# Kernel tuning notes

Measured on AMD Instinct MI355X. Metric: run time of the kernel, lower is better.

Reference implementation:

```python
import jax, jax.numpy as jnp
import numpy as np

N = 50000
E = 800000
D_IN = 128
D_HID = 512
D_OUT = 128
BN_EPS = 1e-5


def setup_inputs() -> dict:
    key = jax.random.key(0)
    ks = jax.random.split(key, 12)
    inp = {}
    inp["v"] = jax.random.normal(ks[0], (N, D_IN), dtype=jnp.float32)
    inp["src"] = jax.random.randint(ks[1], (E,), 0, N, dtype=jnp.int32)
    inp["dst"] = jax.random.randint(ks[2], (E,), 0, N, dtype=jnp.int32)
    inp["edge_weight"] = jax.random.uniform(ks[3], (E,), dtype=jnp.float32)
    # learned parameters
    inp["epsilon"] = jnp.zeros((1, 1), dtype=jnp.float32)  # nn.Parameter([[0.0]])
    s1 = 1.0 / np.sqrt(D_IN)
    s2 = 1.0 / np.sqrt(D_HID)
    inp["W1"] = jax.random.uniform(ks[4], (D_IN, D_HID), minval=-s1, maxval=s1, dtype=jnp.float32)
    inp["b1"] = jax.random.uniform(ks[5], (D_HID,), minval=-s1, maxval=s1, dtype=jnp.float32)
    inp["gamma1"] = jnp.ones((D_HID,), dtype=jnp.float32)
    inp["beta1"] = jnp.zeros((D_HID,), dtype=jnp.float32)
    inp["W2"] = jax.random.uniform(ks[6], (D_HID, D_OUT), minval=-s2, maxval=s2, dtype=jnp.float32)
    inp["b2"] = jax.random.uniform(ks[7], (D_OUT,), minval=-s2, maxval=s2, dtype=jnp.float32)
    inp["gamma2"] = jnp.ones((D_OUT,), dtype=jnp.float32)
    inp["beta2"] = jnp.zeros((D_OUT,), dtype=jnp.float32)
    return inp


def _batchnorm(x, gamma, beta):
    # training-mode BN: batch mean / biased variance over the node axis
    mean = jnp.mean(x, axis=0)
    var = jnp.mean(jnp.square(x - mean), axis=0)
    return gamma * (x - mean) * jax.lax.rsqrt(var + BN_EPS) + beta


def reference(v, src, dst, edge_weight, epsilon, W1, b1, gamma1, beta1, W2, b2, gamma2, beta2):
    n = v.shape[0]
    # sparse.mm(a, v): out[dst] += w * v[src]
    msgs = v[src] * edge_weight[:, None]               # [E, D_IN]
    v_agg = jax.ops.segment_sum(msgs, dst, num_segments=n)  # [N, D_IN]
    v_agg = v_agg + epsilon * v                        # epsilon residual
    h = jax.nn.relu(_batchnorm(v_agg @ W1 + b1, gamma1, beta1))
    out = jax.nn.relu(_batchnorm(h @ W2 + b2, gamma2, beta2))
    return out
```

## Files before the change

### kernel.cpp

```cpp
#include <hip/hip_runtime.h>

#define N_NODES 50000
#define E_EDGES 800000
#define D_INF   128
#define D_HIDF  512
#define D_OUTF  128
#define SCAN_NB ((N_NODES + 255) / 256)
#define M1BLKS  ((N_NODES + 255) / 256)
#define FBLKS   ((N_NODES + 63) / 64)
#define EQ8     (E_EDGES / 8)

#define HIST_NB  ((EQ8 + 255) / 256)
#define CAST_NB  3125
#define PREPW_NB 256
#define PREP_ALL_NB (HIST_NB + CAST_NB + 2 * PREPW_NB)

typedef unsigned short u16;
typedef __attribute__((ext_vector_type(8))) short short8;
typedef __attribute__((ext_vector_type(4))) float floatx4;
typedef const __attribute__((address_space(1))) void gas_t;
typedef __attribute__((address_space(3))) void las_t;

__device__ __forceinline__ u16 f2bf(float f) {
    union { float f; unsigned u; } v; v.f = f;
    unsigned r = (v.u + 0x7fffu + ((v.u >> 16) & 1u)) >> 16;
    return (u16)r;
}
__device__ __forceinline__ float bf2f(u16 b) {
    union { unsigned u; float f; } v; v.u = ((unsigned)b) << 16; return v.f;
}

__global__ __launch_bounds__(256) void prep_all_kernel(
        const float* __restrict__ v, const float* __restrict__ W1,
        const float* __restrict__ W2, const int* __restrict__ dst,
        u16* __restrict__ vbf, u16* __restrict__ W1t, u16* __restrict__ W2t,
        int* __restrict__ counts, int* __restrict__ pos) {
    int b = blockIdx.x;
    int tid = threadIdx.x;
    if (b < HIST_NB) {
        int t = b * 256 + tid;
        if (t >= EQ8) return;
        int d[8], p[8];
#pragma unroll
        for (int k = 0; k < 8; ++k) d[k] = dst[t + k * EQ8];
#pragma unroll
        for (int k = 0; k < 8; ++k) p[k] = atomicAdd(&counts[d[k]], 1);
#pragma unroll
        for (int k = 0; k < 8; ++k) pos[t + k * EQ8] = p[k];
    } else if (b < HIST_NB + CAST_NB) {
        int i = (b - HIST_NB) * 256 + tid;
        const float4 a = ((const float4*)v)[i * 2];
        const float4 c = ((const float4*)v)[i * 2 + 1];
        u16 o[8];
        o[0] = f2bf(a.x); o[1] = f2bf(a.y); o[2] = f2bf(a.z); o[3] = f2bf(a.w);
        o[4] = f2bf(c.x); o[5] = f2bf(c.y); o[6] = f2bf(c.z); o[7] = f2bf(c.w);
        ((float4*)vbf)[i] = *(const float4*)o;
    } else if (b < HIST_NB + CAST_NB + PREPW_NB) {
        int idx = (b - HIST_NB - CAST_NB) * 256 + tid;
        int k1 = idx >> 9, n1 = idx & 511;
        W1t[n1 * 128 + k1] = f2bf(W1[idx]);
    } else {
        int idx = (b - HIST_NB - CAST_NB - PREPW_NB) * 256 + tid;
        int k2 = idx >> 7, n2 = idx & 127;
        W2t[n2 * 512 + k2] = f2bf(W2[idx]);
    }
}

__global__ __launch_bounds__(256) void reduce_kernel(const int* __restrict__ counts,
                                                     int* __restrict__ block_sums) {
    __shared__ int lsum[4];
    int tid = threadIdx.x;
    int gid = blockIdx.x * 256 + tid;
    int s = (gid < N_NODES) ? counts[gid] : 0;
#pragma unroll
    for (int off = 32; off; off >>= 1) s += __shfl_down(s, off);
    if ((tid & 63) == 0) lsum[tid >> 6] = s;
    __syncthreads();
    if (tid == 0) block_sums[blockIdx.x] = lsum[0] + lsum[1] + lsum[2] + lsum[3];
}

__global__ __launch_bounds__(256) void scan_final(const int* __restrict__ counts,
                                                  const int* __restrict__ block_sums,
                                                  int* __restrict__ row_start) {
    __shared__ int sh[256];
    __shared__ int bs[256];
    int tid = threadIdx.x;
    int gid = blockIdx.x * 256 + tid;
    sh[tid] = (gid < N_NODES) ? counts[gid] : 0;
    bs[tid] = (tid < SCAN_NB) ? block_sums[tid] : 0;
    __syncthreads();
    for (int off = 1; off < 256; off <<= 1) {
        int t1 = (tid >= off) ? sh[tid - off] : 0;
        int t2 = (tid >= off) ? bs[tid - off] : 0;
        __syncthreads();
        sh[tid] += t1;
        bs[tid] += t2;
        __syncthreads();
    }
    int boff = (blockIdx.x == 0) ? 0 : bs[blockIdx.x - 1];
    int excl = (tid == 0) ? 0 : sh[tid - 1];
    if (gid < N_NODES) row_start[gid] = boff + excl;
    if (gid == 0) row_start[N_NODES] = E_EDGES;
}

__global__ void fill_kernel(const int* __restrict__ src, const int* __restrict__ dst,
                            const float* __restrict__ w, const int* __restrict__ pos,
                            const int* __restrict__ row_start,
                            int2* __restrict__ csr_ew) {
    int e = blockIdx.x * blockDim.x + threadIdx.x;
    if (e >= E_EDGES) return;
    int d = dst[e];
    int idx = row_start[d] + pos[e];
    int2 rec;
    rec.x = src[e];
    rec.y = __float_as_int(w[e]);
    csr_ew[idx] = rec;
}

__global__ __launch_bounds__(256) void gather_kernel(const u16* __restrict__ vbf,
                                                     const int* __restrict__ row_start,
                                                     const int2* __restrict__ csr_ew,
                                                     const float* __restrict__ eps_p,
                                                     u16* __restrict__ vagg) {
    int node = blockIdx.x * 16 + (threadIdx.x >> 4);
    if (node >= N_NODES) return;
    int c8 = (threadIdx.x & 15) << 3;
    int beg = row_start[node];
    int end = row_start[node + 1];
    float a[8] = {};
    int j = beg;
    for (; j + 1 < end; j += 2) {
        int2 e0 = csr_ew[j];
        int2 e1 = csr_ew[j + 1];
        float w0 = __int_as_float(e0.y);
        float w1 = __int_as_float(e1.y);
        float4 r0 = *(const float4*)(vbf + (size_t)e0.x * D_INF + c8);
        float4 r1 = *(const float4*)(vbf + (size_t)e1.x * D_INF + c8);
        const u16* p0 = (const u16*)&r0;
        const u16* p1 = (const u16*)&r1;
#pragma unroll
        for (int t = 0; t < 8; ++t) a[t] += w0 * bf2f(p0[t]);
#pragma unroll
        for (int t = 0; t < 8; ++t) a[t] += w1 * bf2f(p1[t]);
    }
    if (j < end) {
        int2 e0 = csr_ew[j];
        float w0 = __int_as_float(e0.y);
        float4 r0 = *(const float4*)(vbf + (size_t)e0.x * D_INF + c8);
        const u16* p0 = (const u16*)&r0;
#pragma unroll
        for (int t = 0; t < 8; ++t) a[t] += w0 * bf2f(p0[t]);
    }
    float e = eps_p[0];
    float4 rn = *(const float4*)(vbf + (size_t)node * D_INF + c8);
    const u16* pn = (const u16*)&rn;
    u16 o[8];
#pragma unroll
    for (int t = 0; t < 8; ++t) o[t] = f2bf(a[t] + e * bf2f(pn[t]));
    *(float4*)(vagg + (size_t)node * D_INF + c8) = *(const float4*)o;
}

__global__ __launch_bounds__(512) void stats_gemm1(
        const u16* __restrict__ A, const u16* __restrict__ Bt,
        const float* __restrict__ bias,
        float* __restrict__ psum, float* __restrict__ psq, int M) {
    __shared__ __align__(16) char smem[24576];
    u16* As = (u16*)smem;
    u16* Bs = (u16*)(smem + 16384);
    const int bm = blockIdx.y * 256;
    const int bn = blockIdx.x * 128;
    const int tid = threadIdx.x;
    const int wave = tid >> 6, lane = tid & 63;
    const int wr = wave >> 1, wc = wave & 1;
    const int wm = wr * 64, wn = wc * 64;
    const int lm = lane & 15, quad = lane >> 4;
    floatx4 acc[4][4] = {};
    for (int ks = 0; ks < 4; ++ks) {
        const int k0 = ks << 5;
        {
            const int sub = lane >> 2, s = lane & 3;
#pragma unroll
            for (int t = 0; t < 3; ++t) {
                int ch = wave * 3 + t;
                if (ch < 16) {
                    int row = ch * 16 + sub;
                    int grow = bm + row; if (grow > M - 1) grow = M - 1;
                    int ss = s ^ (row & 3);
                    __builtin_amdgcn_global_load_lds(
                        (gas_t*)(A + (size_t)grow * 128 + k0 + ss * 8),
                        (las_t*)(As + row * 32 + s * 8), 16, 0, 0);
                } else {
                    int row = (ch - 16) * 16 + sub;
                    int ss = s ^ (row & 3);
                    __builtin_amdgcn_global_load_lds(
                        (gas_t*)(Bt + (size_t)(bn + row) * 128 + k0 + ss * 8),
                        (las_t*)(Bs + row * 32 + s * 8), 16, 0, 0);
                }
            }
        }
        __syncthreads();
        short8 af[4], bfr[4];
#pragma unroll
        for (int i = 0; i < 4; ++i) {
            int row = wm + i * 16 + lm;
            af[i] = *(const short8*)&As[row * 32 + ((quad ^ (row & 3)) * 8)];
        }
#pragma unroll
        for (int j = 0; j < 4; ++j) {
            int row = wn + j * 16 + lm;
            bfr[j] = *(const short8*)&Bs[row * 32 + ((quad ^ (row & 3)) * 8)];
        }
#pragma unroll
        for (int i = 0; i < 4; ++i)
#pragma unroll
            for (int j = 0; j < 4; ++j)
                acc[i][j] = __builtin_amdgcn_mfma_f32_16x16x32_bf16(af[i], bfr[j], acc[i][j], 0, 0, 0);
        __syncthreads();
    }
    float* redS = (float*)smem;
    float* redQ = redS + 128;
    if (tid < 128) { redS[tid] = 0.f; redQ[tid] = 0.f; }
    __syncthreads();
#pragma unroll
    for (int j = 0; j < 4; ++j) {
        int cl = wn + j * 16 + lm;
        float bj = bias[bn + cl];
        float s = 0.f, q = 0.f;
#pragma unroll
        for (int i = 0; i < 4; ++i) {
            int row0 = bm + wm + i * 16 + quad * 4;
#pragma unroll
            for (int r = 0; r < 4; ++r)
                if (row0 + r < M) { float x = acc[i][j][r] + bj; s += x; q += x * x; }
        }
        s += __shfl_xor(s, 16); q += __shfl_xor(q, 16);
        s += __shfl_xor(s, 32); q += __shfl_xor(q, 32);
        if (quad == 0) { atomicAdd(&redS[cl], s); atomicAdd(&redQ[cl], q); }
    }
    __syncthreads();
    if (tid < 128) {
        psum[(size_t)blockIdx.y * 512 + bn + tid] = redS[tid];
        psq [(size_t)blockIdx.y * 512 + bn + tid] = redQ[tid];
    }
}

__global__ __launch_bounds__(512, 4) void fused_mlp(
        const u16* __restrict__ vagg, const u16* __restrict__ W1t,
        const u16* __restrict__ W2t,
        const float* __restrict__ b1, const float* __restrict__ scale1,
        const float* __restrict__ shift1, const float* __restrict__ b2,
        u16* __restrict__ x2, float* __restrict__ psum, float* __restrict__ psq,
        int M) {
    __shared__ __align__(16) char smem[81920];
    u16* As  = (u16*)smem;
    u16* W1s = (u16*)(smem + 16384);
    u16* W2s = (u16*)smem;
    u16* hs  = (u16*)(smem + 16384);
    const int bm = blockIdx.x * 64;
    const int tid = threadIdx.x;
    const int wave = tid >> 6, lane = tid & 63;
    const int wr = wave >> 2, wc = wave & 3;
    const int wm = wr * 32;
    const int wn1 = wc * 128;
    const int wn2 = wc * 32;
    const int lm = lane & 15, quad = lane >> 4;

    floatx4 acc1[2][8] = {};
    floatx4 acc2[2][2] = {};

    auto stage_w1 = [&](int win) {
#pragma unroll
        for (int u = 0; u < 8; ++u) {
            int c = tid + u * 512;
            int col = c >> 3, s = c & 7;
            __builtin_amdgcn_global_load_lds(
                (gas_t*)(W1t + (size_t)col * 128 + win * 64 + ((s ^ (col & 7)) * 8)),
                (las_t*)(W1s + col * 64 + s * 8), 16, 0, 0);
        }
    };
    auto stage_w2 = [&](int win) {
#pragma unroll
        for (int u = 0; u < 2; ++u) {
            int c = tid + u * 512;
            int n = c >> 3, s = c & 7;
            __builtin_amdgcn_global_load_lds(
                (gas_t*)(W2t + (size_t)n * 512 + win * 64 + ((s ^ (n & 7)) * 8)),
                (las_t*)(W2s + n * 64 + s * 8), 16, 0, 0);
        }
    };
    auto compute1 = [&](int ks) {
        short8 a[2], b[8];
#pragma unroll
        for (int i = 0; i < 2; ++i) {
            int row = wm + i * 16 + lm;
            a[i] = *(const short8*)&As[row * 128 + (((ks * 4 + quad) ^ (row & 7)) * 8)];
        }
#pragma unroll
        for (int j = 0; j < 8; ++j) {
            int col = wn1 + j * 16 + lm;
            b[j] = *(const short8*)&W1s[col * 64 + ((((ks & 1) * 4 + quad) ^ (col & 7)) * 8)];
        }
#pragma unroll
        for (int i = 0; i < 2; ++i)
#pragma unroll
            for (int j = 0; j < 8; ++j)
                acc1[i][j] = __builtin_amdgcn_mfma_f32_16x16x32_bf16(a[i], b[j], acc1[i][j], 0, 0, 0);
    };
    auto compute2 = [&](int ks) {
        short8 a[2], b[2];
#pragma unroll
        for (int i = 0; i < 2; ++i) {
            int row = wm + i * 16 + lm;
            a[i] = *(const short8*)&hs[row * 512 + (((ks * 4 + quad) ^ (row & 7)) * 8)];
        }
#pragma unroll
        for (int j = 0; j < 2; ++j) {
            int n = wn2 + j * 16 + lm;
            b[j] = *(const short8*)&W2s[n * 64 + ((((ks & 1) * 4 + quad) ^ (n & 7)) * 8)];
        }
#pragma unroll
        for (int i = 0; i < 2; ++i)
#pragma unroll
            for (int j = 0; j < 2; ++j)
                acc2[i][j] = __builtin_amdgcn_mfma_f32_16x16x32_bf16(a[i], b[j], acc2[i][j], 0, 0, 0);
    };

#pragma unroll
    for (int u = 0; u < 2; ++u) {
        int c = tid + u * 512;
        int row = c >> 4, s = c & 15;
        int grow = bm + row; if (grow > M - 1) grow = M - 1;
        __builtin_amdgcn_global_load_lds(
            (gas_t*)(vagg + (size_t)grow * 128 + ((s ^ (row & 7)) * 8)),
            (las_t*)(As + row * 128 + s * 8), 16, 0, 0);
    }
    stage_w1(0);
    __syncthreads();
    compute1(0); compute1(1);
    __syncthreads();
    stage_w1(1);
    __syncthreads();
    compute1(2); compute1(3);
    __syncthreads();

    stage_w2(0);
    {
        float hsc[8], hsh[8];
#pragma unroll
        for (int j = 0; j < 8; ++j) {
            int col = wn1 + j * 16 + lm;
            float sc = scale1[col];
            hsc[j] = sc;
            hsh[j] = shift1[col] + sc * b1[col];
        }
#pragma unroll
        for (int i = 0; i < 2; ++i)
#pragma unroll
            for (int j = 0; j < 8; ++j)
#pragma unroll
                for (int r = 0; r < 4; ++r) {
                    int row = wm + i * 16 + quad * 4 + r;
                    int col = wn1 + j * 16 + lm;
                    float hv = fmaxf(0.f, acc1[i][j][r] * hsc[j] + hsh[j]);
                    hs[row * 512 + (((col >> 3) ^ (row & 7)) * 8) + (col & 7)] = f2bf(hv);
                }
    }
    __syncthreads();

#pragma unroll
    for (int win = 0; win < 8; ++win) {
        compute2(win * 2); compute2(win * 2 + 1);
        __syncthreads();
        if (win < 7) { stage_w2(win + 1); __syncthreads(); }
    }

    float* redS = (float*)smem;
    float* redQ = redS + 128;
    if (tid < 128) { redS[tid] = 0.f; redQ[tid] = 0.f; }
    __syncthreads();
    float bj2[2];
#pragma unroll
    for (int j = 0; j < 2; ++j) {
        int cl = wn2 + j * 16 + lm;
        bj2[j] = b2[cl];
        float s = 0.f, q = 0.f;
#pragma unroll
        for (int i = 0; i < 2; ++i) {
            int row0 = bm + wm + i * 16 + quad * 4;
#pragma unroll
            for (int r = 0; r < 4; ++r)
                if (row0 + r < M) { float x = acc2[i][j][r] + bj2[j]; s += x; q += x * x; }
        }
        s += __shfl_xor(s, 16); q += __shfl_xor(q, 16);
        s += __shfl_xor(s, 32); q += __shfl_xor(q, 32);
        if (quad == 0) { atomicAdd(&redS[cl], s); atomicAdd(&redQ[cl], q); }
    }
    __syncthreads();
    if (tid < 128) {
        psum[(size_t)blockIdx.x * 128 + tid] = redS[tid];
        psq [(size_t)blockIdx.x * 128 + tid] = redQ[tid];
    }
    __syncthreads();

    float* obuf = (float*)smem;
#pragma unroll
    for (int i = 0; i < 2; ++i)
#pragma unroll
        for (int j = 0; j < 2; ++j)
#pragma unroll
            for (int r = 0; r < 4; ++r) {
                int row = wm + i * 16 + quad * 4 + r;
                int col = wn2 + j * 16 + lm;
                obuf[row * 132 + col] = acc2[i][j][r] + bj2[j];
            }
    __syncthreads();
    {
        int row = tid >> 3, seg = (tid & 7) * 16;
        int grow = bm + row;
        if (grow < M) {
            u16 ob[16];
#pragma unroll
            for (int t = 0; t < 4; ++t) {
                float4 f = *(float4*)&obuf[row * 132 + seg + t * 4];
                ob[t * 4 + 0] = f2bf(f.x);
                ob[t * 4 + 1] = f2bf(f.y);
                ob[t * 4 + 2] = f2bf(f.z);
                ob[t * 4 + 3] = f2bf(f.w);
            }
            u16* dp = x2 + (size_t)grow * 128 + seg;
            *(float4*)dp       = *(float4*)ob;
            *(float4*)(dp + 8) = *(float4*)(ob + 8);
        }
    }
}

__global__ __launch_bounds__(1024) void bn_finalize_kernel(
        const float* __restrict__ psum, const float* __restrict__ psq,
        const float* __restrict__ gamma, const float* __restrict__ beta,
        float* __restrict__ scale, float* __restrict__ shift,
        int nblocks, int Ncols, float inv_n) {
    __shared__ float shS[16][64];
    __shared__ float shQ[16][64];
    const int tx = threadIdx.x;
    const int ty = threadIdx.y;
    const int c = blockIdx.x * 64 + tx;
    float s = 0.f, q = 0.f;
    for (int b = ty; b < nblocks; b += 16) {
        s += psum[(size_t)b * Ncols + c];
        q += psq [(size_t)b * Ncols + c];
    }
    shS[ty][tx] = s;
    shQ[ty][tx] = q;
    __syncthreads();
    if (ty == 0) {
        float S = 0.f, Q = 0.f;
#pragma unroll
        for (int r = 0; r < 16; ++r) { S += shS[r][tx]; Q += shQ[r][tx]; }
        float m = S * inv_n;
        float var = Q * inv_n - m * m;
        float rs = rsqrtf(var + 1e-5f);
        float sc = gamma[c] * rs;
        scale[c] = sc;
        shift[c] = beta[c] - sc * m;
    }
}

__global__ void bn2_apply_kernel(const u16* __restrict__ X, float* __restrict__ Y,
                                 const float* __restrict__ scale,
                                 const float* __restrict__ shift, int n8) {
    int i = blockIdx.x * blockDim.x + threadIdx.x;
    if (i >= n8) return;
    int c = (i & 15) << 3;
    float4 raw = ((const float4*)X)[i];
    const u16* xb = (const u16*)&raw;
    float4 sc0 = *(const float4*)(scale + c);
    float4 sc1 = *(const float4*)(scale + c + 4);
    float4 sh0 = *(const float4*)(shift + c);
    float4 sh1 = *(const float4*)(shift + c + 4);
    float4 y0, y1;
    y0.x = fmaxf(0.f, bf2f(xb[0]) * sc0.x + sh0.x);
    y0.y = fmaxf(0.f, bf2f(xb[1]) * sc0.y + sh0.y);
    y0.z = fmaxf(0.f, bf2f(xb[2]) * sc0.z + sh0.z);
    y0.w = fmaxf(0.f, bf2f(xb[3]) * sc0.w + sh0.w);
    y1.x = fmaxf(0.f, bf2f(xb[4]) * sc1.x + sh1.x);
    y1.y = fmaxf(0.f, bf2f(xb[5]) * sc1.y + sh1.y);
    y1.z = fmaxf(0.f, bf2f(xb[6]) * sc1.z + sh1.z);
    y1.w = fmaxf(0.f, bf2f(xb[7]) * sc1.w + sh1.w);
    ((float4*)Y)[i * 2]     = y0;
    ((float4*)Y)[i * 2 + 1] = y1;
}

extern "C" void kernel_launch(void* const* d_in, const int* in_sizes, int n_in,
                              void* d_out, int out_size, void* d_ws, size_t ws_size,
                              hipStream_t stream) {
    const float* v    = (const float*)d_in[0];
    const int* src    = (const int*)d_in[1];
    const int* dst    = (const int*)d_in[2];
    const float* ew   = (const float*)d_in[3];
    const float* eps  = (const float*)d_in[4];
    const float* W1   = (const float*)d_in[5];
    const float* b1   = (const float*)d_in[6];
    const float* g1   = (const float*)d_in[7];
    const float* be1  = (const float*)d_in[8];
    const float* W2   = (const float*)d_in[9];
    const float* b2   = (const float*)d_in[10];
    const float* g2   = (const float*)d_in[11];
    const float* be2  = (const float*)d_in[12];
    float* out = (float*)d_out;

    char* base = (char*)d_ws;
    u16* vbf  = (u16*)(base + 51200000ull);
    u16* vagg = (u16*)(base + 64000000ull);
    u16* x2   = (u16*)(base + 76800000ull);
    u16* W1t  = (u16*)(base + 89600000ull);
    u16* W2t  = (u16*)(base + 89731072ull);
    float* psum   = (float*)(base + 89862144ull);
    float* psq    = (float*)(base + 90663168ull);
    float* scale1 = (float*)(base + 91464192ull);
    float* shift1 = scale1 + 512;
    float* scale2 = shift1 + 512;
    float* shift2 = scale2 + 128;
    int* counts     = (int*)(shift2 + 128);
    int* row_start  = counts + 50000;
    int* pos        = row_start + 50004;
    int2* csr_ew    = (int2*)(pos + 800000);
    int* block_sums = (int*)(csr_ew + 800000);

    hipMemsetAsync(counts, 0, (size_t)50000 * sizeof(int), stream);

    prep_all_kernel<<<PREP_ALL_NB, 256, 0, stream>>>(v, W1, W2, dst, vbf, W1t, W2t,
                                                     counts, pos);
    reduce_kernel<<<SCAN_NB, 256, 0, stream>>>(counts, block_sums);
    scan_final<<<SCAN_NB, 256, 0, stream>>>(counts, block_sums, row_start);
    fill_kernel<<<(E_EDGES + 255) / 256, 256, 0, stream>>>(src, dst, ew, pos, row_start, csr_ew);
    gather_kernel<<<(N_NODES + 15) / 16, 256, 0, stream>>>(vbf, row_start, csr_ew, eps, vagg);

    {
        dim3 grid(D_HIDF / 128, M1BLKS);
        stats_gemm1<<<grid, 512, 0, stream>>>(vagg, W1t, b1, psum, psq, N_NODES);
    }
    bn_finalize_kernel<<<D_HIDF / 64, dim3(64, 16), 0, stream>>>(
        psum, psq, g1, be1, scale1, shift1, M1BLKS, D_HIDF, 1.0f / N_NODES);

    fused_mlp<<<FBLKS, 512, 0, stream>>>(vagg, W1t, W2t, b1, scale1, shift1, b2,
                                         x2, psum, psq, N_NODES);
    bn_finalize_kernel<<<D_OUTF / 64, dim3(64, 16), 0, stream>>>(
        psum, psq, g2, be2, scale2, shift2, FBLKS, D_OUTF, 1.0f / N_NODES);

    {
        int n8 = N_NODES * D_OUTF / 8;
        bn2_apply_kernel<<<(n8 + 255) / 256, 256, 0, stream>>>(x2, out, scale2, shift2, n8);
    }
}
```

Before: 278.8 us.

## Compute BN1 statistics via Gram matrix of aggregated features instead of GEMM

Replaces the first-layer statistics GEMM (N x 128 times 128 x 512) with a Gram matrix G = vagg^T vagg (128x128) plus column sums, then derives per-channel mean and variance of vagg@W1+b1 algebraically as w^T G w and w·colsum. This cuts the MFMA work for the stats pass by roughly 4x and removes the W1 loads there. It adds a partial-Gram reduction kernel and a small finalize kernel. The E[x^2]-m^2 formulation in fp32 may lose some precision relative to the direct computation.

```diff
diff --git a/kernel.cpp b/kernel.cpp
--- a/kernel.cpp
+++ b/kernel.cpp
@@ -6,7 +6,7 @@
 #define D_HIDF  512
 #define D_OUTF  128
 #define SCAN_NB ((N_NODES + 255) / 256)
-#define M1BLKS  ((N_NODES + 255) / 256)
+#define GBLKS   196
 #define FBLKS   ((N_NODES + 63) / 64)
 #define EQ8     (E_EDGES / 8)
 
@@ -160,87 +160,109 @@
     *(float4*)(vagg + (size_t)node * D_INF + c8) = *(const float4*)o;
 }
 
-__global__ __launch_bounds__(512) void stats_gemm1(
-        const u16* __restrict__ A, const u16* __restrict__ Bt,
-        const float* __restrict__ bias,
-        float* __restrict__ psum, float* __restrict__ psq, int M) {
-    __shared__ __align__(16) char smem[24576];
-    u16* As = (u16*)smem;
-    u16* Bs = (u16*)(smem + 16384);
-    const int bm = blockIdx.y * 256;
-    const int bn = blockIdx.x * 128;
+__global__ __launch_bounds__(512) void gram_kernel(
+        const u16* __restrict__ vagg,
+        float* __restrict__ Gp, float* __restrict__ csp, int M) {
+    __shared__ __align__(16) char smem[16384];
+    u16* vT = (u16*)smem;
     const int tid = threadIdx.x;
     const int wave = tid >> 6, lane = tid & 63;
-    const int wr = wave >> 1, wc = wave & 1;
-    const int wm = wr * 64, wn = wc * 64;
     const int lm = lane & 15, quad = lane >> 4;
-    floatx4 acc[4][4] = {};
-    for (int ks = 0; ks < 4; ++ks) {
-        const int k0 = ks << 5;
-        {
-            const int sub = lane >> 2, s = lane & 3;
-#pragma unroll
-            for (int t = 0; t < 3; ++t) {
-                int ch = wave * 3 + t;
-                if (ch < 16) {
-                    int row = ch * 16 + sub;
-                    int grow = bm + row; if (grow > M - 1) grow = M - 1;
-                    int ss = s ^ (row & 3);
-                    __builtin_amdgcn_global_load_lds(
-                        (gas_t*)(A + (size_t)grow * 128 + k0 + ss * 8),
-                        (las_t*)(As + row * 32 + s * 8), 16, 0, 0);
-                } else {
-                    int row = (ch - 16) * 16 + sub;
-                    int ss = s ^ (row & 3);
-                    __builtin_amdgcn_global_load_lds(
-                        (gas_t*)(Bt + (size_t)(bn + row) * 128 + k0 + ss * 8),
-                        (las_t*)(Bs + row * 32 + s * 8), 16, 0, 0);
-                }
-            }
-        }
+    const int bm = blockIdx.x * 256;
+    const int r0 = tid >> 4;
+    const int c8 = tid & 15;
+    floatx4 acc[8] = {};
+    float csum[8] = {};
+#pragma unroll
+    for (int ck = 0; ck < 8; ++ck) {
+        int grow = bm + ck * 32 + r0;
+        float4 rv = make_float4(0.f, 0.f, 0.f, 0.f);
+        if (grow < M) rv = *(const float4*)(vagg + (size_t)grow * 128 + c8 * 8);
+        const u16* pv = (const u16*)&rv;
         __syncthreads();
-        short8 af[4], bfr[4];
-#pragma unroll
-        for (int i = 0; i < 4; ++i) {
-            int row = wm + i * 16 + lm;
-            af[i] = *(const short8*)&As[row * 32 + ((quad ^ (row & 3)) * 8)];
-        }
-#pragma unroll
-        for (int j = 0; j < 4; ++j) {
-            int row = wn + j * 16 + lm;
-            bfr[j] = *(const short8*)&Bs[row * 32 + ((quad ^ (row & 3)) * 8)];
-        }
-#pragma unroll
-        for (int i = 0; i < 4; ++i)
-#pragma unroll
-            for (int j = 0; j < 4; ++j)
-                acc[i][j] = __builtin_amdgcn_mfma_f32_16x16x32_bf16(af[i], bfr[j], acc[i][j], 0, 0, 0);
+#pragma unroll
+        for (int j = 0; j < 8; ++j) {
+            vT[(c8 * 8 + j) * 40 + r0] = pv[j];
+            csum[j] += bf2f(pv[j]);
+        }
         __syncthreads();
-    }
-    float* redS = (float*)smem;
-    float* redQ = redS + 128;
-    if (tid < 128) { redS[tid] = 0.f; redQ[tid] = 0.f; }
-    __syncthreads();
-#pragma unroll
-    for (int j = 0; j < 4; ++j) {
-        int cl = wn + j * 16 + lm;
-        float bj = bias[bn + cl];
-        float s = 0.f, q = 0.f;
-#pragma unroll
-        for (int i = 0; i < 4; ++i) {
-            int row0 = bm + wm + i * 16 + quad * 4;
-#pragma unroll
-            for (int r = 0; r < 4; ++r)
-                if (row0 + r < M) { float x = acc[i][j][r] + bj; s += x; q += x * x; }
-        }
-        s += __shfl_xor(s, 16); q += __shfl_xor(q, 16);
-        s += __shfl_xor(s, 32); q += __shfl_xor(q, 32);
-        if (quad == 0) { atomicAdd(&redS[cl], s); atomicAdd(&redQ[cl], q); }
-    }
+        short8 af = *(const short8*)&vT[(wave * 16 + lm) * 40 + quad * 8];
+#pragma unroll
+        for (int tj = 0; tj < 8; ++tj) {
+            short8 bf = *(const short8*)&vT[(tj * 16 + lm) * 40 + quad * 8];
+            acc[tj] = __builtin_amdgcn_mfma_f32_16x16x32_bf16(af, bf, acc[tj], 0, 0, 0);
+        }
+    }
+    __syncthreads();
+#pragma unroll
+    for (int tj = 0; tj < 8; ++tj)
+#pragma unroll
+        for (int r = 0; r < 4; ++r) {
+            int gi = wave * 16 + quad * 4 + r;
+            int gj = tj * 16 + lm;
+            Gp[(size_t)blockIdx.x * 16384 + gi * 128 + gj] = acc[tj][r];
+        }
+    float* cred = (float*)smem;
+#pragma unroll
+    for (int j = 0; j < 8; ++j) cred[r0 * 128 + c8 * 8 + j] = csum[j];
     __syncthreads();
     if (tid < 128) {
-        psum[(size_t)blockIdx.y * 512 + bn + tid] = redS[tid];
-        psq [(size_t)blockIdx.y * 512 + bn + tid] = redQ[tid];
+        float s = 0.f;
+#pragma unroll
+        for (int r = 0; r < 32; ++r) s += cred[r * 128 + tid];
+        csp[(size_t)blockIdx.x * 128 + tid] = s;
+    }
+}
+
+__global__ __launch_bounds__(256) void gsum_kernel(
+        const float* __restrict__ Gp, const float* __restrict__ csp,
+        float* __restrict__ G, float* __restrict__ colsum) {
+    int i = blockIdx.x * 256 + threadIdx.x;
+    if (i < 16384) {
+        float s = 0.f;
+        for (int b = 0; b < GBLKS; ++b) s += Gp[(size_t)b * 16384 + i];
+        G[i] = s;
+    } else if (i < 16384 + 128) {
+        int c = i - 16384;
+        float s = 0.f;
+        for (int b = 0; b < GBLKS; ++b) s += csp[(size_t)b * 128 + c];
+        colsum[c] = s;
+    }
+}
+
+__global__ __launch_bounds__(128) void bn1fin_gram(
+        const float* __restrict__ G, const float* __restrict__ colsum,
+        const u16* __restrict__ W1t, const float* __restrict__ b1,
+        const float* __restrict__ g1, const float* __restrict__ be1,
+        float* __restrict__ scale1, float* __restrict__ shift1) {
+    __shared__ float red[4];
+    const int c = blockIdx.x;
+    const int i = threadIdx.x;
+    float wi = bf2f(W1t[c * 128 + i]);
+    float dot = 0.f;
+    for (int j = 0; j < 128; ++j)
+        dot += G[j * 128 + i] * bf2f(W1t[c * 128 + j]);
+    float qp = wi * dot;
+    float sp = wi * colsum[i];
+#pragma unroll
+    for (int off = 32; off; off >>= 1) {
+        qp += __shfl_down(qp, off);
+        sp += __shfl_down(sp, off);
+    }
+    if ((i & 63) == 0) { red[(i >> 6) * 2] = qp; red[(i >> 6) * 2 + 1] = sp; }
+    __syncthreads();
+    if (i == 0) {
+        float q = red[0] + red[2];
+        float s = red[1] + red[3];
+        float b = b1[c];
+        const float inv_n = 1.0f / (float)N_NODES;
+        float m = s * inv_n + b;
+        float ex2 = (q + 2.f * b * s) * inv_n + b * b;
+        float var = ex2 - m * m;
+        float rs = rsqrtf(var + 1e-5f);
+        float sc = g1[c] * rs;
+        scale1[c] = sc;
+        shift1[c] = be1[c] - sc * m;
     }
 }
 
@@ -509,6 +531,10 @@
     float* out = (float*)d_out;
 
     char* base = (char*)d_ws;
+    float* Gp     = (float*)(base);
+    float* csp    = (float*)(base + 13000000ull);
+    float* G      = (float*)(base + 13200000ull);
+    float* colsum = (float*)(base + 13300000ull);
     u16* vbf  = (u16*)(base + 51200000ull);
     u16* vagg = (u16*)(base + 64000000ull);
     u16* x2   = (u16*)(base + 76800000ull);
@@ -535,12 +561,9 @@
     fill_kernel<<<(E_EDGES + 255) / 256, 256, 0, stream>>>(src, dst, ew, pos, row_start, csr_ew);
     gather_kernel<<<(N_NODES + 15) / 16, 256, 0, stream>>>(vbf, row_start, csr_ew, eps, vagg);
 
-    {
-        dim3 grid(D_HIDF / 128, M1BLKS);
-        stats_gemm1<<<grid, 512, 0, stream>>>(vagg, W1t, b1, psum, psq, N_NODES);
-    }
-    bn_finalize_kernel<<<D_HIDF / 64, dim3(64, 16), 0, stream>>>(
-        psum, psq, g1, be1, scale1, shift1, M1BLKS, D_HIDF, 1.0f / N_NODES);
+    gram_kernel<<<GBLKS, 512, 0, stream>>>(vagg, Gp, csp, N_NODES);
+    gsum_kernel<<<(16384 + 128 + 255) / 256, 256, 0, stream>>>(Gp, csp, G, colsum);
+    bn1fin_gram<<<D_HIDF, 128, 0, stream>>>(G, colsum, W1t, b1, g1, be1, scale1, shift1);
 
     fused_mlp<<<FBLKS, 512, 0, stream>>>(vagg, W1t, W2t, b1, scale1, shift1, b2,
                                          x2, psum, psq, N_NODES);
```

Measured after the change: 285.3 us. 2.3% more time.

## Halve fused MLP shared memory by splitting hidden into two passes

Applied to the files above, without the earlier changes.

Shrinks the fused MLP kernel's LDS from 80KB to 48KB. W1 is now staged in 32-wide K windows (four stages instead of two), and the hidden activations are written and consumed in two 256-column halves, each followed by its own set of W2 windows. The goal is to fit more blocks per CU and raise occupancy. In exchange there are more barriers and staging rounds, with fewer MFMAs between each synchronisation.

```diff
diff --git a/kernel.cpp b/kernel.cpp
--- a/kernel.cpp
+++ b/kernel.cpp
@@ -251,7 +251,7 @@
         const float* __restrict__ shift1, const float* __restrict__ b2,
         u16* __restrict__ x2, float* __restrict__ psum, float* __restrict__ psq,
         int M) {
-    __shared__ __align__(16) char smem[81920];
+    __shared__ __align__(16) char smem[49152];
     u16* As  = (u16*)smem;
     u16* W1s = (u16*)(smem + 16384);
     u16* W2s = (u16*)smem;
@@ -270,35 +270,35 @@
 
     auto stage_w1 = [&](int win) {
 #pragma unroll
-        for (int u = 0; u < 8; ++u) {
+        for (int u = 0; u < 4; ++u) {
             int c = tid + u * 512;
-            int col = c >> 3, s = c & 7;
+            int col = c >> 2, s = c & 3;
             __builtin_amdgcn_global_load_lds(
-                (gas_t*)(W1t + (size_t)col * 128 + win * 64 + ((s ^ (col & 7)) * 8)),
-                (las_t*)(W1s + col * 64 + s * 8), 16, 0, 0);
+                (gas_t*)(W1t + (size_t)col * 128 + win * 32 + ((s ^ (col & 3)) * 8)),
+                (las_t*)(W1s + col * 32 + s * 8), 16, 0, 0);
         }
     };
-    auto stage_w2 = [&](int win) {
+    auto stage_w2 = [&](int p, int w) {
 #pragma unroll
         for (int u = 0; u < 2; ++u) {
             int c = tid + u * 512;
             int n = c >> 3, s = c & 7;
             __builtin_amdgcn_global_load_lds(
-                (gas_t*)(W2t + (size_t)n * 512 + win * 64 + ((s ^ (n & 7)) * 8)),
+                (gas_t*)(W2t + (size_t)n * 512 + w * 128 + p * 64 + ((s ^ (n & 7)) * 8)),
                 (las_t*)(W2s + n * 64 + s * 8), 16, 0, 0);
         }
     };
-    auto compute1 = [&](int ks) {
+    auto compute1 = [&](int win) {
         short8 a[2], b[8];
 #pragma unroll
         for (int i = 0; i < 2; ++i) {
             int row = wm + i * 16 + lm;
-            a[i] = *(const short8*)&As[row * 128 + (((ks * 4 + quad) ^ (row & 7)) * 8)];
+            a[i] = *(const short8*)&As[row * 128 + (((win * 4 + quad) ^ (row & 7)) * 8)];
         }
 #pragma unroll
         for (int j = 0; j < 8; ++j) {
             int col = wn1 + j * 16 + lm;
-            b[j] = *(const short8*)&W1s[col * 64 + ((((ks & 1) * 4 + quad) ^ (col & 7)) * 8)];
+            b[j] = *(const short8*)&W1s[col * 32 + ((quad ^ (col & 3)) * 8)];
         }
 #pragma unroll
         for (int i = 0; i < 2; ++i)
@@ -306,23 +306,44 @@
             for (int j = 0; j < 8; ++j)
                 acc1[i][j] = __builtin_amdgcn_mfma_f32_16x16x32_bf16(a[i], b[j], acc1[i][j], 0, 0, 0);
     };
-    auto compute2 = [&](int ks) {
+    auto compute2 = [&](int w, int ks) {
         short8 a[2], b[2];
 #pragma unroll
         for (int i = 0; i < 2; ++i) {
             int row = wm + i * 16 + lm;
-            a[i] = *(const short8*)&hs[row * 512 + (((ks * 4 + quad) ^ (row & 7)) * 8)];
+            a[i] = *(const short8*)&hs[row * 256 + (((w * 8 + ks * 4 + quad) ^ (row & 7)) * 8)];
         }
 #pragma unroll
         for (int j = 0; j < 2; ++j) {
             int n = wn2 + j * 16 + lm;
-            b[j] = *(const short8*)&W2s[n * 64 + ((((ks & 1) * 4 + quad) ^ (n & 7)) * 8)];
+            b[j] = *(const short8*)&W2s[n * 64 + (((ks * 4 + quad) ^ (n & 7)) * 8)];
         }
 #pragma unroll
         for (int i = 0; i < 2; ++i)
 #pragma unroll
             for (int j = 0; j < 2; ++j)
                 acc2[i][j] = __builtin_amdgcn_mfma_f32_16x16x32_bf16(a[i], b[j], acc2[i][j], 0, 0, 0);
+    };
+    auto store_h = [&](int p) {
+        float hsc[4], hsh[4];
+#pragma unroll
+        for (int j = 0; j < 4; ++j) {
+            int col = wn1 + (p * 4 + j) * 16 + lm;
+            float sc = scale1[col];
+            hsc[j] = sc;
+            hsh[j] = shift1[col] + sc * b1[col];
+        }
+#pragma unroll
+        for (int i = 0; i < 2; ++i)
+#pragma unroll
+            for (int j = 0; j < 4; ++j)
+#pragma unroll
+                for (int r = 0; r < 4; ++r) {
+                    int row = wm + i * 16 + quad * 4 + r;
+                    int kp = wc * 64 + j * 16 + lm;
+                    float hv = fmaxf(0.f, acc1[i][p * 4 + j][r] * hsc[j] + hsh[j]);
+                    hs[row * 256 + (((kp >> 3) ^ (row & 7)) * 8) + (kp & 7)] = f2bf(hv);
+                }
     };
 
 #pragma unroll
@@ -336,42 +357,32 @@
     }
     stage_w1(0);
     __syncthreads();
-    compute1(0); compute1(1);
+    compute1(0);
     __syncthreads();
     stage_w1(1);
     __syncthreads();
-    compute1(2); compute1(3);
-    __syncthreads();
-
-    stage_w2(0);
-    {
-        float hsc[8], hsh[8];
-#pragma unroll
-        for (int j = 0; j < 8; ++j) {
-            int col = wn1 + j * 16 + lm;
-            float sc = scale1[col];
-            hsc[j] = sc;
-            hsh[j] = shift1[col] + sc * b1[col];
-        }
-#pragma unroll
-        for (int i = 0; i < 2; ++i)
-#pragma unroll
-            for (int j = 0; j < 8; ++j)
-#pragma unroll
-                for (int r = 0; r < 4; ++r) {
-                    int row = wm + i * 16 + quad * 4 + r;
-                    int col = wn1 + j * 16 + lm;
-                    float hv = fmaxf(0.f, acc1[i][j][r] * hsc[j] + hsh[j]);
-                    hs[row * 512 + (((col >> 3) ^ (row & 7)) * 8) + (col & 7)] = f2bf(hv);
-                }
-    }
-    __syncthreads();
-
-#pragma unroll
-    for (int win = 0; win < 8; ++win) {
-        compute2(win * 2); compute2(win * 2 + 1);
+    compute1(1);
+    __syncthreads();
+    stage_w1(2);
+    __syncthreads();
+    compute1(2);
+    __syncthreads();
+    stage_w1(3);
+    __syncthreads();
+    compute1(3);
+    __syncthreads();
+
+#pragma unroll
+    for (int p = 0; p < 2; ++p) {
+        stage_w2(p, 0);
+        store_h(p);
         __syncthreads();
-        if (win < 7) { stage_w2(win + 1); __syncthreads(); }
+#pragma unroll
+        for (int w = 0; w < 4; ++w) {
+            compute2(w, 0); compute2(w, 1);
+            __syncthreads();
+            if (w < 3) { stage_w2(p, w + 1); __syncthreads(); }
+        }
     }
 
     float* redS = (float*)smem;
```

New measurement: 270.3 us, median of 2. 1.03x faster.
